# Optimization experiments

Measured on AMD Instinct MI355X. Metric: run time of the kernel, lower is better.

Reference implementation:

```python
import jax, jax.numpy as jnp
import numpy as np

KERNEL_MUL = 2.0
KERNEL_NUM = 5


def _mmd(source, target, kernel_mul=KERNEL_MUL, kernel_num=KERNEL_NUM, fix_sigma=None):
    n = source.shape[0]
    total = jnp.concatenate([source, target], axis=0)  # [2N, D]
    n_samples = total.shape[0]
    # Pairwise squared L2 distances via Gram matrix (same math as the
    # broadcasted (2N,2N,D) diff-square-sum, but O(N^2 D) GEMM instead).
    sq = jnp.sum(total * total, axis=1)                # [2N]
    gram = total @ total.T                             # [2N, 2N]
    L2 = sq[:, None] + sq[None, :] - 2.0 * gram        # [2N, 2N]
    if fix_sigma:
        bandwidth = fix_sigma
    else:
        # torch used L2_distance.data -> detached; match with stop_gradient
        bandwidth = jax.lax.stop_gradient(jnp.sum(L2)) / (n_samples ** 2 - n_samples)
    bandwidth = bandwidth / (kernel_mul ** (kernel_num // 2))
    kernels = jnp.zeros_like(L2)
    for i in range(kernel_num):
        kernels = kernels + jnp.exp(-L2 / (bandwidth * kernel_mul ** i))
    XX = kernels[:n, :n]
    YY = kernels[n:, n:]
    XY = kernels[:n, n:]
    YX = kernels[n:, :n]
    return jnp.mean(XX + YY - XY - YX)


def setup_inputs() -> dict:
    key = jax.random.key(0)
    k1, k2 = jax.random.split(key)
    N, D = 4096, 512
    source = jax.random.normal(k1, (N, D), dtype=jnp.float32)
    target = jax.random.normal(k2, (N, D), dtype=jnp.float32)
    return {"source": source, "target": target}


def reference(source, target):
    # MMD_sample_size = inf >= batch_size -> single full-batch MMD
    return _mmd(source, target)
```

## Files before the change

kernel.cpp:

```cpp
#include <hip/hip_runtime.h>
#include <hip/hip_fp16.h>


#define NS 8192
#define D_DIM 512
#define NTILE 32
#define NBLK 528
#define PBLK 512

typedef _Float16 f16x8 __attribute__((ext_vector_type(8)));
typedef float f32x4 __attribute__((ext_vector_type(4)));

__global__ __launch_bounds__(256) void prep(const float* __restrict__ src,
                                            const float* __restrict__ tgt,
                                            __half* __restrict__ Th,
                                            float* __restrict__ sq,
                                            float* __restrict__ colp,
                                            float* __restrict__ sqp) {
    __shared__ float lcs[4][D_DIM];
    __shared__ float wsq[4];
    int tid = threadIdx.x, w = tid >> 6, l = tid & 63;
    int r0 = blockIdx.x * 16 + w * 4;
    float cs[8];
#pragma unroll
    for (int j = 0; j < 8; ++j) cs[j] = 0.f;
    float ws = 0.f;

#pragma unroll
    for (int rr = 0; rr < 4; ++rr) {
        int r = r0 + rr;
        const float* rowp = (r < 4096) ? (src + (size_t)r * D_DIM)
                                       : (tgt + (size_t)(r - 4096) * D_DIM);
        float4 v0 = *reinterpret_cast<const float4*>(rowp + l * 8);
        float4 v1 = *reinterpret_cast<const float4*>(rowp + l * 8 + 4);
        float f[8] = {v0.x, v0.y, v0.z, v0.w, v1.x, v1.y, v1.z, v1.w};
        __half h[8];
        float s = 0.f;
#pragma unroll
        for (int j = 0; j < 8; ++j) {
            h[j] = __float2half(f[j]);
            float fj = __half2float(h[j]);
            s += fj * fj;
            cs[j] += fj;
        }
        *reinterpret_cast<int4*>(Th + (size_t)r * D_DIM + l * 8) =
            *reinterpret_cast<const int4*>(h);
#pragma unroll
        for (int off = 32; off; off >>= 1) s += __shfl_xor(s, off, 64);
        if (l == 0) { sq[r] = s; ws += s; }
    }
    if (l == 0) wsq[w] = ws;
#pragma unroll
    for (int j = 0; j < 8; ++j) lcs[w][l * 8 + j] = cs[j];
    __syncthreads();
#pragma unroll
    for (int j = 0; j < 2; ++j) {
        int c = j * 256 + tid;
        colp[(size_t)blockIdx.x * D_DIM + c] =
            (lcs[0][c] + lcs[1][c]) + (lcs[2][c] + lcs[3][c]);
    }
    if (tid == 0) sqp[blockIdx.x] = (wsq[0] + wsq[1]) + (wsq[2] + wsq[3]);
}

__global__ __launch_bounds__(512) void combine(const float* __restrict__ colp,
                                               const float* __restrict__ sqp,
                                               float* __restrict__ Sacc,
                                               float* __restrict__ Cacc) {
    __shared__ float red[512];
    __shared__ float red2[512];
    int t = threadIdx.x;
    float s = 0.f;
#pragma unroll 16
    for (int b = 0; b < PBLK; ++b) s += colp[(size_t)b * D_DIM + t];
    float sv = sqp[t];
    red[t] = s * s; red2[t] = sv; __syncthreads();
    for (int off = 256; off; off >>= 1) {
        if (t < off) { red[t] += red[t + off]; red2[t] += red2[t + off]; }
        __syncthreads();
    }
    if (t == 0) { Cacc[0] = red[0]; Sacc[0] = red2[0]; }
}

__global__ __launch_bounds__(512, 2) void mmd_main(const __half* __restrict__ Th,
                                                   const float* __restrict__ sq,
                                                   const float* __restrict__ Sacc,
                                                   const float* __restrict__ Cacc,
                                                   float* __restrict__ partials) {
    __shared__ __half Ah[2][256 * 64];
    __shared__ __half Bh[2][256 * 64];
    __shared__ float wred[8];

    int borig = blockIdx.x;
    int b = (borig & 7) * (NBLK / 8) + (borig >> 3);
    int ti = 0, rem = b;
    while (rem >= NTILE - ti) { rem -= NTILE - ti; ++ti; }
    int tj = ti + rem;
    int ibase = ti * 256, jbase = tj * 256;
    float wgt = ((ti == tj) ? 1.f : 2.f) * (((ti < 16) == (tj < 16)) ? 1.f : -1.f);

    int tid = threadIdx.x;
    int wid = tid >> 6, lane = tid & 63;
    int wm = wid >> 2, wn = wid & 3;
    int cl = lane >> 4;

    double S = (double)Sacc[0];
    double C = (double)Cacc[0];

    f32x4 acc[8][4];
#pragma unroll
    for (int m = 0; m < 8; ++m)
#pragma unroll
        for (int n = 0; n < 4; ++n) acc[m][n] = f32x4{0.f, 0.f, 0.f, 0.f};

    auto STAGE = [&](int buf, int k0) {
#pragma unroll
        for (int it = 0; it < 4; ++it) {
            int h16 = tid + it * 512;
            int row = h16 >> 3, ch = h16 & 7;
            int scol = ((ch ^ (row & 7)) * 8);
            __builtin_amdgcn_global_load_lds(
                (const __attribute__((address_space(1))) unsigned int*)(Th + (size_t)(ibase + row) * D_DIM + k0 + scol),
                (__attribute__((address_space(3))) unsigned int*)(&Ah[buf][h16 * 8]), 16, 0, 0);
            __builtin_amdgcn_global_load_lds(
                (const __attribute__((address_space(1))) unsigned int*)(Th + (size_t)(jbase + row) * D_DIM + k0 + scol),
                (__attribute__((address_space(3))) unsigned int*)(&Bh[buf][h16 * 8]), 16, 0, 0);
        }
    };

    auto COMPUTE = [&](int buf) {
#pragma unroll
        for (int ks = 0; ks < 2; ++ks) {
            f16x8 afr[8], bfr[4];
#pragma unroll
            for (int m = 0; m < 8; ++m) {
                int ra = wm * 128 + m * 16 + (lane & 15);
                int pc = (ks * 4 + cl) ^ (ra & 7);
                afr[m] = *reinterpret_cast<const f16x8*>(&Ah[buf][ra * 64 + pc * 8]);
            }
#pragma unroll
            for (int n = 0; n < 4; ++n) {
                int rb = wn * 64 + n * 16 + (lane & 15);
                int pc = (ks * 4 + cl) ^ (rb & 7);
                bfr[n] = *reinterpret_cast<const f16x8*>(&Bh[buf][rb * 64 + pc * 8]);
            }
#pragma unroll
            for (int m = 0; m < 8; ++m)
#pragma unroll
                for (int n = 0; n < 4; ++n)
                    acc[m][n] = __builtin_amdgcn_mfma_f32_16x16x32_f16(afr[m], bfr[n], acc[m][n], 0, 0, 0);
        }
    };

    STAGE(0, 0);
#pragma unroll
    for (int t = 0; t < 7; ++t) {
        STAGE((t + 1) & 1, (t + 1) * 64);
        asm volatile("s_waitcnt vmcnt(8)" ::: "memory");
        __builtin_amdgcn_s_barrier();
        COMPUTE(t & 1);
        asm volatile("" ::: "memory");
        __builtin_amdgcn_s_barrier();
    }
    asm volatile("s_waitcnt vmcnt(0)" ::: "memory");
    __builtin_amdgcn_s_barrier();
    COMPUTE(1);

    double sumL2 = 2.0 * (double)NS * S - 2.0 * C;
    double bwv = sumL2 / ((double)NS * NS - (double)NS) / 4.0;
    float c0s = (float)(-1.4426950408889634 / (bwv * 16.0));
    float m2c0s = -2.f * c0s;

    float sci[32], scj[4];
#pragma unroll
    for (int m = 0; m < 8; ++m)
#pragma unroll
        for (int r = 0; r < 4; ++r)
            sci[m * 4 + r] = sq[ibase + wm * 128 + m * 16 + (lane >> 4) * 4 + r] * c0s;
#pragma unroll
    for (int n = 0; n < 4; ++n)
        scj[n] = sq[jbase + wn * 64 + n * 16 + (lane & 15)] * c0s;

    float ksum = 0.f;
#pragma unroll
    for (int m = 0; m < 8; ++m)
#pragma unroll
        for (int n = 0; n < 4; ++n)
#pragma unroll
            for (int r = 0; r < 4; ++r) {
                float x4 = fmaf(acc[m][n][r], m2c0s, sci[m * 4 + r] + scj[n]);
                float e4 = __builtin_amdgcn_exp2f(x4);
                float e3 = e4 * e4;
                float e2 = e3 * e3;
                float e1 = e2 * e2;
                float e0 = e1 * e1;
                ksum += ((e4 + e3) + (e2 + e1)) + e0;
            }
#pragma unroll
    for (int off = 32; off; off >>= 1) ksum += __shfl_xor(ksum, off, 64);
    if (lane == 0) wred[wid] = ksum;
    __syncthreads();
    if (tid == 0) {
        float tot = ((wred[0] + wred[1]) + (wred[2] + wred[3]))
                  + ((wred[4] + wred[5]) + (wred[6] + wred[7]));
        partials[borig] = tot * wgt;
    }
}

__global__ void finalize(const float* __restrict__ partials, float* __restrict__ out) {
    __shared__ double red[256];
    int t = threadIdx.x;
    double s = 0.0;
    for (int i = t; i < NBLK; i += 256) s += (double)partials[i];
    red[t] = s; __syncthreads();
    for (int off = 128; off; off >>= 1) { if (t < off) red[t] += red[t + off]; __syncthreads(); }
    if (t == 0) out[0] = (float)(red[0] * (1.0 / (4096.0 * 4096.0)));
}

extern "C" void kernel_launch(void* const* d_in, const int* in_sizes, int n_in,
                              void* d_out, int out_size, void* d_ws, size_t ws_size,
                              hipStream_t stream) {
    (void)in_sizes; (void)n_in; (void)out_size; (void)ws_size;
    const float* src = (const float*)d_in[0];
    const float* tgt = (const float*)d_in[1];
    char* ws = (char*)d_ws;
    __half* Th      = (__half*)ws;
    float* sq       = (float*)(ws + 8388608);
    float* colp     = (float*)(ws + 8421376);
    float* sqp      = (float*)(ws + 9469952);
    float* Sacc     = (float*)(ws + 9472000);
    float* Cacc     = (float*)(ws + 9472004);
    float* partials = (float*)(ws + 9472008);
    float* out      = (float*)d_out;

    hipLaunchKernelGGL(prep, dim3(PBLK), dim3(256), 0, stream, src, tgt, Th, sq, colp, sqp);
    hipLaunchKernelGGL(combine, dim3(1), dim3(512), 0, stream, colp, sqp, Sacc, Cacc);
    hipLaunchKernelGGL(mmd_main, dim3(NBLK), dim3(512), 0, stream, Th, sq, Sacc, Cacc, partials);
    hipLaunchKernelGGL(finalize, dim3(1), dim3(256), 0, stream, partials, out);
}
```

Baseline: 144.4 us.

## Interleave LDS fragment loads, global prefetch and MFMA in four-phase pipeline

Restructures the GEMM main loop into four phases per K-tile, each loading half of the A fragments (and B fragments as needed) from LDS and then issuing 16 MFMAs. Global-to-LDS prefetch of the next tile is split across phases, and sched_barrier, s_setprio and extra barriers pin the instruction order. This halves the A-fragment registers, which could relieve register pressure, and aims for finer overlap of memory and matrix work. In exchange it adds many more barriers per tile and waits for the full prefetch at the end of each tile.

```diff
diff --git a/kernel.cpp b/kernel.cpp
--- a/kernel.cpp
+++ b/kernel.cpp
@@ -112,58 +112,95 @@
 #pragma unroll
         for (int n = 0; n < 4; ++n) acc[m][n] = f32x4{0.f, 0.f, 0.f, 0.f};
 
-    auto STAGE = [&](int buf, int k0) {
-#pragma unroll
-        for (int it = 0; it < 4; ++it) {
-            int h16 = tid + it * 512;
-            int row = h16 >> 3, ch = h16 & 7;
-            int scol = ((ch ^ (row & 7)) * 8);
-            __builtin_amdgcn_global_load_lds(
-                (const __attribute__((address_space(1))) unsigned int*)(Th + (size_t)(ibase + row) * D_DIM + k0 + scol),
-                (__attribute__((address_space(3))) unsigned int*)(&Ah[buf][h16 * 8]), 16, 0, 0);
-            __builtin_amdgcn_global_load_lds(
-                (const __attribute__((address_space(1))) unsigned int*)(Th + (size_t)(jbase + row) * D_DIM + k0 + scol),
-                (__attribute__((address_space(3))) unsigned int*)(&Bh[buf][h16 * 8]), 16, 0, 0);
+    f16x8 afr[4], bfr[4];
+
+    auto GLOAD2 = [&](int nbuf, int kt, int it) {
+        int h16 = tid + it * 512;
+        int row = h16 >> 3, ch = h16 & 7;
+        int scol = ((ch ^ (row & 7)) * 8);
+        __builtin_amdgcn_global_load_lds(
+            (const __attribute__((address_space(1))) unsigned int*)(Th + (size_t)(ibase + row) * D_DIM + kt * 64 + scol),
+            (__attribute__((address_space(3))) unsigned int*)(&Ah[nbuf][h16 * 8]), 16, 0, 0);
+        __builtin_amdgcn_global_load_lds(
+            (const __attribute__((address_space(1))) unsigned int*)(Th + (size_t)(jbase + row) * D_DIM + kt * 64 + scol),
+            (__attribute__((address_space(3))) unsigned int*)(&Bh[nbuf][h16 * 8]), 16, 0, 0);
+    };
+    auto LOADB = [&](int buf, int ks) {
+#pragma unroll
+        for (int n = 0; n < 4; ++n) {
+            int rb = wn * 64 + n * 16 + (lane & 15);
+            int pc = (ks * 4 + cl) ^ (rb & 7);
+            bfr[n] = *reinterpret_cast<const f16x8*>(&Bh[buf][rb * 64 + pc * 8]);
         }
     };
-
-    auto COMPUTE = [&](int buf) {
-#pragma unroll
-        for (int ks = 0; ks < 2; ++ks) {
-            f16x8 afr[8], bfr[4];
-#pragma unroll
-            for (int m = 0; m < 8; ++m) {
-                int ra = wm * 128 + m * 16 + (lane & 15);
-                int pc = (ks * 4 + cl) ^ (ra & 7);
-                afr[m] = *reinterpret_cast<const f16x8*>(&Ah[buf][ra * 64 + pc * 8]);
-            }
-#pragma unroll
-            for (int n = 0; n < 4; ++n) {
-                int rb = wn * 64 + n * 16 + (lane & 15);
-                int pc = (ks * 4 + cl) ^ (rb & 7);
-                bfr[n] = *reinterpret_cast<const f16x8*>(&Bh[buf][rb * 64 + pc * 8]);
-            }
-#pragma unroll
-            for (int m = 0; m < 8; ++m)
-#pragma unroll
-                for (int n = 0; n < 4; ++n)
-                    acc[m][n] = __builtin_amdgcn_mfma_f32_16x16x32_f16(afr[m], bfr[n], acc[m][n], 0, 0, 0);
+    auto LOADA = [&](int buf, int ks, int half) {
+#pragma unroll
+        for (int m = 0; m < 4; ++m) {
+            int ra = wm * 128 + (half * 4 + m) * 16 + (lane & 15);
+            int pc = (ks * 4 + cl) ^ (ra & 7);
+            afr[m] = *reinterpret_cast<const f16x8*>(&Ah[buf][ra * 64 + pc * 8]);
         }
     };
-
-    STAGE(0, 0);
-#pragma unroll
-    for (int t = 0; t < 7; ++t) {
-        STAGE((t + 1) & 1, (t + 1) * 64);
-        asm volatile("s_waitcnt vmcnt(8)" ::: "memory");
-        __builtin_amdgcn_s_barrier();
-        COMPUTE(t & 1);
-        asm volatile("" ::: "memory");
-        __builtin_amdgcn_s_barrier();
-    }
+    auto DOMFMA = [&](int half) {
+#pragma unroll
+        for (int m = 0; m < 4; ++m)
+#pragma unroll
+            for (int n = 0; n < 4; ++n)
+                acc[half * 4 + m][n] =
+                    __builtin_amdgcn_mfma_f32_16x16x32_f16(afr[m], bfr[n], acc[half * 4 + m][n], 0, 0, 0);
+    };
+
+#pragma unroll
+    for (int it = 0; it < 4; ++it) GLOAD2(0, 0, it);
     asm volatile("s_waitcnt vmcnt(0)" ::: "memory");
     __builtin_amdgcn_s_barrier();
-    COMPUTE(1);
+    __builtin_amdgcn_sched_barrier(0);
+
+#pragma unroll
+    for (int t = 0; t < 8; ++t) {
+        int buf = t & 1, nbuf = buf ^ 1;
+        LOADB(buf, 0);
+        LOADA(buf, 0, 0);
+        if (t < 7) { GLOAD2(nbuf, t + 1, 0); GLOAD2(nbuf, t + 1, 1); }
+        __builtin_amdgcn_s_barrier();
+        asm volatile("s_waitcnt lgkmcnt(0)" ::: "memory");
+        __builtin_amdgcn_sched_barrier(0);
+        __builtin_amdgcn_s_setprio(1);
+        DOMFMA(0);
+        __builtin_amdgcn_s_setprio(0);
+        __builtin_amdgcn_s_barrier();
+        __builtin_amdgcn_sched_barrier(0);
+        LOADA(buf, 0, 1);
+        if (t < 7) { GLOAD2(nbuf, t + 1, 2); GLOAD2(nbuf, t + 1, 3); }
+        __builtin_amdgcn_s_barrier();
+        asm volatile("s_waitcnt lgkmcnt(0)" ::: "memory");
+        __builtin_amdgcn_sched_barrier(0);
+        __builtin_amdgcn_s_setprio(1);
+        DOMFMA(1);
+        __builtin_amdgcn_s_setprio(0);
+        __builtin_amdgcn_s_barrier();
+        __builtin_amdgcn_sched_barrier(0);
+        LOADB(buf, 1);
+        LOADA(buf, 1, 0);
+        __builtin_amdgcn_s_barrier();
+        asm volatile("s_waitcnt lgkmcnt(0)" ::: "memory");
+        __builtin_amdgcn_sched_barrier(0);
+        __builtin_amdgcn_s_setprio(1);
+        DOMFMA(0);
+        __builtin_amdgcn_s_setprio(0);
+        __builtin_amdgcn_s_barrier();
+        __builtin_amdgcn_sched_barrier(0);
+        LOADA(buf, 1, 1);
+        __builtin_amdgcn_s_barrier();
+        asm volatile("s_waitcnt lgkmcnt(0)" ::: "memory");
+        __builtin_amdgcn_sched_barrier(0);
+        __builtin_amdgcn_s_setprio(1);
+        DOMFMA(1);
+        __builtin_amdgcn_s_setprio(0);
+        if (t < 7) asm volatile("s_waitcnt vmcnt(0)" ::: "memory");
+        __builtin_amdgcn_s_barrier();
+        __builtin_amdgcn_sched_barrier(0);
+    }
 
     double sumL2 = 2.0 * (double)NS * S - 2.0 * C;
     double bwv = sumL2 / ((double)NS * NS - (double)NS) / 4.0;
```

Result: slower. 153.9 us (+6.6%).
